# Kernel tuning notes

Measured on AMD Instinct MI355X. Metric: run time of the kernel, lower is better.

The kernel has to match this reference:

```python
import jax, jax.numpy as jnp
from jax import lax
import numpy as np

DN = ('NCDHW', 'OIDHW', 'NCDHW')
EPS = 1e-3  # BatchNorm1d eps=0.001
GRID = (41, 512, 512)  # spatial_shape [40,512,512] + [1,0,0]


def _block(x, mask, w, gamma, beta, rmean, rvar, stride, padding):
    # Regular (non-submanifold) sparse conv computes the same values as a dense
    # conv on the zero-filled grid; active OUTPUT sites are exactly those reached
    # by any active input site through the kernel window. BN+ReLU act only on
    # active sites (inactive sites stay exactly 0), hence the mask multiply.
    y = lax.conv_general_dilated(x, w, stride, padding, dimension_numbers=DN)
    k1 = jnp.ones((1, 1) + w.shape[2:], x.dtype)
    m = lax.conv_general_dilated(mask, k1, stride, padding, dimension_numbers=DN)
    m = (m > 0).astype(x.dtype)
    inv = gamma / jnp.sqrt(rvar + EPS)
    scale = inv.reshape(1, -1, 1, 1, 1)
    shift = (beta - rmean * inv).reshape(1, -1, 1, 1, 1)
    return jax.nn.relu(y * scale + shift) * m, m


def setup_inputs() -> dict:
    key = jax.random.key(0)
    NV, B = 120000, 2
    kf, kb, kz, ky, kx, kp = jax.random.split(key, 6)
    voxel_features = jax.random.normal(kf, (NV, 3), jnp.float32)
    coors = jnp.stack([
        jax.random.randint(kb, (NV,), 0, B, jnp.int32),
        jax.random.randint(kz, (NV,), 0, 40, jnp.int32),
        jax.random.randint(ky, (NV,), 0, 512, jnp.int32),
        jax.random.randint(kx, (NV,), 0, 512, jnp.int32)], axis=1)
    inp = {"voxel_features": voxel_features, "coors": coors, "batch_size": B}
    chans = [(3, 16, (3, 3, 3)), (16, 32, (3, 3, 3)), (32, 64, (3, 3, 3)), (64, 64, (3, 1, 1))]
    for i, (ci, co, k) in enumerate(chans, 1):
        kw, kg, kbb, km, kv = jax.random.split(jax.random.fold_in(kp, i), 5)
        fan = ci * k[0] * k[1] * k[2]
        inp[f"w{i}"] = jax.random.normal(kw, (co, ci) + k, jnp.float32) / np.sqrt(fan).astype(np.float32)
        inp[f"g{i}"] = jax.random.uniform(kg, (co,), jnp.float32, 0.5, 1.5)
        inp[f"bb{i}"] = jax.random.normal(kbb, (co,), jnp.float32) * 0.1
        inp[f"rm{i}"] = jax.random.normal(km, (co,), jnp.float32) * 0.1
        inp[f"rv{i}"] = jax.random.uniform(kv, (co,), jnp.float32, 0.5, 1.5)
    return inp


def reference(voxel_features, coors, batch_size,
              w1, g1, bb1, rm1, rv1,
              w2, g2, bb2, rm2, rv2,
              w3, g3, bb3, rm3, rv3,
              w4, g4, bb4, rm4, rv4):
    D, H, W = GRID
    C = voxel_features.shape[1]
    b, z, y, x = coors[:, 0], coors[:, 1], coors[:, 2], coors[:, 3]
    dense = jnp.zeros((batch_size, C, D, H, W), voxel_features.dtype)
    dense = dense.at[b, :, z, y, x].add(voxel_features)  # scatter voxels to grid
    mask = jnp.zeros((batch_size, 1, D, H, W), voxel_features.dtype).at[b, 0, z, y, x].set(1.0)
    h, m = _block(dense, mask, w1, g1, bb1, rm1, rv1, (2, 2, 2), [(1, 1), (1, 1), (1, 1)])
    h, m = _block(h, m, w2, g2, bb2, rm2, rv2, (2, 2, 2), [(1, 1), (1, 1), (1, 1)])
    h, m = _block(h, m, w3, g3, bb3, rm3, rv3, (2, 2, 2), [(0, 0), (1, 1), (1, 1)])
    h, m = _block(h, m, w4, g4, bb4, rm4, rv4, (2, 1, 1), [(0, 0), (0, 0), (0, 0)])
    N, Co, Dd, Hh, Ww = h.shape  # [B, 64, 2, 64, 64]
    return h.reshape(N, Co * Dd, Hh, Ww)
```

## Files before the change

### kernel.cpp

```cpp
#include <hip/hip_runtime.h>

#define EPS 1e-3f


static __device__ __forceinline__ unsigned f2bf(float f) {
    unsigned u = __float_as_uint(f);
    return (u + 0x7FFFu + ((u >> 16) & 1u)) >> 16;
}

typedef _Float16 f16x8 __attribute__((ext_vector_type(8)));
typedef float f32x4 __attribute__((ext_vector_type(4)));
typedef float f32x16 __attribute__((ext_vector_type(16)));

#define SLACK_BYTE 2752512
#define SLACK_Y1   90832912

__global__ __launch_bounds__(256) void repack_prezero(
    const float* __restrict__ g1, const float* __restrict__ b1,
    const float* __restrict__ rm1, const float* __restrict__ rv1,
    const float* __restrict__ w2, const float* __restrict__ g2, const float* __restrict__ b2,
    const float* __restrict__ rm2, const float* __restrict__ rv2,
    const float* __restrict__ w3, const float* __restrict__ g3, const float* __restrict__ b3,
    const float* __restrict__ rm3, const float* __restrict__ rv3,
    const float* __restrict__ w4, const float* __restrict__ g4, const float* __restrict__ b4,
    const float* __restrict__ rm4, const float* __restrict__ rv4,
    _Float16* __restrict__ wB2, _Float16* __restrict__ wB3,
    _Float16* __restrict__ wB4, float* __restrict__ shb,
    const int* __restrict__ coors, int NV, unsigned short* __restrict__ y1,
    unsigned char* __restrict__ m1, float* __restrict__ m3)
{
    if (blockIdx.x >= 1034) {
        const int i = (blockIdx.x - 1034) * 256 + threadIdx.x;
        if (i < NV) {
            const int b = coors[4 * i + 0];
            const int z = coors[4 * i + 1];
            const int y = coors[4 * i + 2];
            const int x = coors[4 * i + 3];
            int ozv[2], nz = 0, oyv[2], ny = 0, oxv[2], nx = 0;
#pragma unroll
            for (int k = 0; k < 3; ++k) {
                int t = z + 1 - k;
                if (t >= 0 && !(t & 1)) { int o = t >> 1; if (o < 21) ozv[nz++] = o; }
            }
#pragma unroll
            for (int k = 0; k < 3; ++k) {
                int t = y + 1 - k;
                if (t >= 0 && !(t & 1)) { int o = t >> 1; if (o < 256) oyv[ny++] = o; }
            }
#pragma unroll
            for (int k = 0; k < 3; ++k) {
                int t = x + 1 - k;
                if (t >= 0 && !(t & 1)) { int o = t >> 1; if (o < 256) oxv[nx++] = o; }
            }
            const uint4 zz = {0u, 0u, 0u, 0u};
            for (int a = 0; a < nz; ++a)
                for (int bb = 0; bb < ny; ++bb)
                    for (int c = 0; c < nx; ++c) {
                        const int sp = ozv[a] * 65536 + oyv[bb] * 256 + oxv[c];
                        uint4* p = (uint4*)(y1 + (size_t)(b * 1376256 + sp) * 16);
                        p[0] = zz;
                        p[1] = zz;
                    }
        }
        asm volatile("s_waitcnt vmcnt(0)" ::: "memory");
        return;
    }
    if (blockIdx.x >= 321) {
        const int idx16 = (blockIdx.x - 321) * 256 + threadIdx.x;
        const uint4 zz = {0u, 0u, 0u, 0u};
        if (idx16 < 172034) {
            ((uint4*)m1)[idx16] = zz;
        } else if (idx16 < 182274) {
            ((uint4*)m3)[idx16 - 172034] = zz;
        }
        return;
    }

    const int i = blockIdx.x * 256 + threadIdx.x;
    if (i < 13824) {
        const int j = i & 7, lane = (i >> 3) & 63, tap = i >> 9;
        const int oc = lane & 31;
        const int cin = (lane >> 5) * 8 + j;
        const float inv = g2[oc] * rsqrtf(rv2[oc] + EPS);
        wB2[i] = (_Float16)(w2[(oc * 16 + cin) * 27 + tap] * inv);
    } else if (i >= 14336 && i < 69632) {
        const int j2 = i - 14336;
        const int j = j2 & 7, lane = (j2 >> 3) & 63, t = (j2 >> 9) & 3, tap = j2 >> 11;
        const int q = lane >> 4, n = lane & 15;
        const int oc = t * 16 + n;
        const int cin = q * 8 + j;
        const float inv = g3[oc] * rsqrtf(rv3[oc] + EPS);
        wB3[j2] = (_Float16)(w3[(oc * 32 + cin) * 27 + tap] * inv);
    } else if (i >= 69632 && i < 81920) {
        const int j2 = i - 69632;
        const int j = j2 & 7, lane = (j2 >> 3) & 63, t = (j2 >> 9) & 3, c = j2 >> 11;
        const int q = lane >> 4, n = lane & 15;
        const int oc = t * 16 + n;
        const int k = c * 32 + q * 8 + j;
        const int dz = k >> 6, cin = k & 63;
        const float inv = g4[oc] * rsqrtf(rv4[oc] + EPS);
        wB4[j2] = (_Float16)(w4[(oc * 64 + cin) * 3 + dz] * inv);
    } else if (i >= 81920 && i < 82112) {
        const int j = i - 81920;
        if (j < 32) {
            const float inv = g2[j] * rsqrtf(rv2[j] + EPS);
            shb[j] = b2[j] - rm2[j] * inv;
        } else if (j < 96) {
            const int o = j - 32;
            const float inv = g3[o] * rsqrtf(rv3[o] + EPS);
            shb[j] = b3[o] - rm3[o] * inv;
        } else if (j < 160) {
            const int o = j - 96;
            const float inv = g4[o] * rsqrtf(rv4[o] + EPS);
            shb[j] = b4[o] - rm4[o] * inv;
        } else if (j < 176) {
            const int o = j - 160;
            shb[j] = g1[o] * rsqrtf(rv1[o] + EPS);
        } else if (j < 192) {
            const int o = j - 176;
            const float inv = g1[o] * rsqrtf(rv1[o] + EPS);
            shb[j] = b1[o] - rm1[o] * inv;
        }
    }
}

__global__ __launch_bounds__(256) void scatter_l1(
    const float* __restrict__ vf, const int* __restrict__ coors, int NV,
    const float* __restrict__ w1, const float* __restrict__ shb,
    unsigned short* __restrict__ y1, unsigned char* __restrict__ m1)
{
    __shared__ float ws[16 * 3 * 27];
    for (int e = threadIdx.x; e < 16 * 3 * 27; e += 256)
        ws[e] = w1[e] * shb[160 + e / 81];
    __syncthreads();

    const int gid = blockIdx.x * 256 + threadIdx.x;
    const int i = gid >> 3;
    const int oc2 = gid & 7;
    if (i < NV) {
        const int oc = oc2 * 2;

        const int b = coors[4 * i + 0];
        const int z = coors[4 * i + 1];
        const int y = coors[4 * i + 2];
        const int x = coors[4 * i + 3];
        const float f0 = vf[3 * i + 0];
        const float f1 = vf[3 * i + 1];
        const float f2 = vf[3 * i + 2];

        int ozv[2], kzv[2], nz = 0;
        int oyv[2], kyv[2], ny = 0;
        int oxv[2], kxv[2], nx = 0;
#pragma unroll
        for (int k = 0; k < 3; ++k) {
            int t = z + 1 - k;
            if (t >= 0 && !(t & 1)) { int o = t >> 1; if (o < 21) { ozv[nz] = o; kzv[nz] = k; ++nz; } }
        }
#pragma unroll
        for (int k = 0; k < 3; ++k) {
            int t = y + 1 - k;
            if (t >= 0 && !(t & 1)) { int o = t >> 1; if (o < 256) { oyv[ny] = o; kyv[ny] = k; ++ny; } }
        }
#pragma unroll
        for (int k = 0; k < 3; ++k) {
            int t = x + 1 - k;
            if (t >= 0 && !(t & 1)) { int o = t >> 1; if (o < 256) { oxv[nx] = o; kxv[nx] = k; ++nx; } }
        }

        for (int a = 0; a < nz; ++a)
            for (int bb = 0; bb < ny; ++bb)
                for (int c = 0; c < nx; ++c) {
                    const int oz = ozv[a], oy = oyv[bb], ox = oxv[c];
                    const int tap = (kzv[a] * 3 + kyv[bb]) * 3 + kxv[c];
                    const int sp = oz * 65536 + oy * 256 + ox;
                    if (oc2 == 0) m1[b * 1376256 + sp] = 1;
                    const float s0 = ws[oc * 81 + tap] * f0 + ws[oc * 81 + 27 + tap] * f1 +
                                     ws[oc * 81 + 54 + tap] * f2;
                    const float s1 = ws[(oc + 1) * 81 + tap] * f0 +
                                     ws[(oc + 1) * 81 + 27 + tap] * f1 +
                                     ws[(oc + 1) * 81 + 54 + tap] * f2;
                    const unsigned pk = f2bf(s0) | (f2bf(s1) << 16);
                    unsigned* addr = (unsigned*)(y1 + (size_t)(b * 1376256 + sp) * 16 +
                                                 oc2 * 2);
                    asm volatile("global_atomic_pk_add_bf16 %0, %1, off"
                                 : : "v"(addr), "v"(pk) : "memory");
                }
    }
    asm volatile("s_waitcnt vmcnt(0)" ::: "memory");
}

__global__ __launch_bounds__(256) void masks_pass(
    const unsigned char* __restrict__ m1, float* __restrict__ m2,
    float* __restrict__ m3)
{
    const int idx = blockIdx.x * 256 + threadIdx.x;
    const int b = idx / 180224;
    const int r = idx - b * 180224;
    const int oz = r >> 14, r2 = r & 16383, oy = r2 >> 7, ox = r2 & 127;
    const int iz0 = 2 * oz - 1, iyb = 2 * oy - 1, ixb = 2 * ox - 1;
    unsigned msum = 0;
#pragma unroll
    for (int kz = 0; kz < 3; ++kz) {
        const int iz = iz0 + kz;
#pragma unroll
        for (int ky = 0; ky < 3; ++ky) {
            const int iy = iyb + ky;
#pragma unroll
            for (int kx = 0; kx < 3; ++kx) {
                const int ix = ixb + kx;
                if ((unsigned)iz < 21u && (unsigned)iy < 256u &&
                    (unsigned)ix < 256u)
                    msum |= m1[b * 1376256 + iz * 65536 + iy * 256 + ix];
            }
        }
    }
    m2[idx] = msum ? 1.f : 0.f;

    if (msum) {
        int ozv[2], nz = 0, oyv[2], ny = 0, oxv[2], nx = 0;
#pragma unroll
        for (int k = 0; k < 3; ++k) {
            int t = oz - k;
            if (t >= 0 && !(t & 1)) { int o = t >> 1; if (o < 5) ozv[nz++] = o; }
        }
#pragma unroll
        for (int k = 0; k < 3; ++k) {
            int t = oy + 1 - k;
            if (t >= 0 && !(t & 1)) { int o = t >> 1; if (o < 64) oyv[ny++] = o; }
        }
#pragma unroll
        for (int k = 0; k < 3; ++k) {
            int t = ox + 1 - k;
            if (t >= 0 && !(t & 1)) { int o = t >> 1; if (o < 64) oxv[nx++] = o; }
        }
        for (int a = 0; a < nz; ++a)
            for (int bb = 0; bb < ny; ++bb)
                for (int c = 0; c < nx; ++c)
                    m3[b * 20480 + ozv[a] * 4096 + oyv[bb] * 64 + oxv[c]] = 1.0f;
    }
}

__global__ __launch_bounds__(256) __attribute__((amdgpu_waves_per_eu(4, 8)))
void conv_l2(
    const unsigned char* __restrict__ y1c,
    const unsigned char* __restrict__ m1,
    const uint4* __restrict__ wB2,
    const float* __restrict__ m2, const float* __restrict__ shb,
    _Float16* __restrict__ h2h)
{
    __shared__ unsigned char lds[3 * 8320];

    const int tid = threadIdx.x;
    const int lane = tid & 63;
    const int w = tid >> 6;
    const int m = lane & 31, h = lane >> 5;

    const int sbid = (blockIdx.x & 7) * 352 + (blockIdx.x >> 3);
    const int oy = sbid / 22;
    const int plane = sbid - oy * 22;
    const int b = plane / 11, oz = plane - b * 11;

    const int ox0 = w * 32;
    const int iz0 = 2 * oz - 1, iyb = 2 * oy - 1;
    const int ixm = 2 * (ox0 + m) - 1;
    const int bbase = b * 1376256;
    const int qoff = h * 16;

    unsigned mbits = 0;
#pragma unroll
    for (int t = 0; t < 27; ++t) {
        const int kz = t / 9, ky = (t / 3) % 3, kx = t % 3;
        const int iz = iz0 + kz, iy = iyb + ky, ix = ixm + kx;
        const bool v = (unsigned)iz < 21u && (unsigned)iy < 256u &&
                       (unsigned)ix < 256u;
        const int cell = bbase + iz * 65536 + iy * 256 + ix;
        mbits |= (unsigned)(m1[v ? cell : SLACK_BYTE] & 1) << t;
    }

    float s1v[8];
    {
        const float4* sp = (const float4*)(shb + 176 + h * 8);
        const float4 a0 = sp[0], a1 = sp[1];
        s1v[0] = a0.x; s1v[1] = a0.y; s1v[2] = a0.z; s1v[3] = a0.w;
        s1v[4] = a1.x; s1v[5] = a1.y; s1v[6] = a1.z; s1v[7] = a1.w;
    }

    int rdo[3];
#pragma unroll
    for (int kx = 0; kx < 3; ++kx) {
        const unsigned lx = (unsigned)(2 * (ox0 + m) + kx);
        const unsigned L = lx * 32 + qoff;
        rdo[kx] = (int)(L ^ (((L >> 7) & 7u) << 4));
    }

    int su_row[7], su_ix[7], su_half[7];
#pragma unroll
    for (int it = 0; it < 7; ++it) {
        const int t = it * 256 + tid;
        const int row = t / 520;
        const int u = t - row * 520;
        const unsigned L = (unsigned)(u * 16) ^ (((unsigned)(u >> 3) & 7u) << 4);
        su_row[it] = row;
        su_ix[it] = (int)(L >> 5) - 1;
        su_half[it] = (int)((L >> 4) & 1u);
    }

    f32x16 acc;
#pragma unroll
    for (int r = 0; r < 16; ++r) acc[r] = 0.f;

    for (int kz = 0; kz < 3; ++kz) {
        const int iz = iz0 + kz;
        const bool izok = (unsigned)iz < 21u;
        const int zrow = bbase + iz * 65536;

        __syncthreads();
#pragma unroll
        for (int it = 0; it < 7; ++it) {
            const int t = it * 256 + tid;
            if (t < 1560) {
                const int row = su_row[it];
                const int iy = iyb + row;
                const int ix = su_ix[it];
                const bool v = izok && (unsigned)iy < 256u && (unsigned)ix < 256u;
                const int srcb = v ? ((zrow + iy * 256 + ix) * 32 + su_half[it] * 16)
                                   : (int)SLACK_Y1;
                const int bt = t - lane;
                __builtin_amdgcn_global_load_lds(
                    (const __attribute__((address_space(1))) unsigned char*)(y1c + srcb),
                    (__attribute__((address_space(3))) unsigned char*)(lds + bt * 16),
                    16, 0, 0);
            }
        }
        asm volatile("s_waitcnt vmcnt(0)" ::: "memory");
        __syncthreads();

#pragma unroll
        for (int ky = 0; ky < 3; ++ky) {
            const int rbase = ky * 8320;
#pragma unroll
            for (int kx = 0; kx < 3; ++kx) {
                const int tap = kz * 9 + ky * 3 + kx;
                const uint4 ua = *(const uint4*)(lds + rbase + rdo[kx]);
                const bool act = (mbits >> tap) & 1u;
                unsigned od[4];
                const unsigned dvs[4] = {ua.x, ua.y, ua.z, ua.w};
#pragma unroll
                for (int jj = 0; jj < 4; ++jj) {
                    const unsigned dv = dvs[jj];
                    const float vlo = fmaxf(__uint_as_float(dv << 16) + s1v[2 * jj], 0.f);
                    const float vhi = fmaxf(__uint_as_float(dv & 0xFFFF0000u) + s1v[2 * jj + 1], 0.f);
                    const unsigned pk = __builtin_bit_cast(
                        unsigned, __builtin_amdgcn_cvt_pkrtz(vlo, vhi));
                    od[jj] = act ? pk : 0u;
                }
                const uint4 uc = {od[0], od[1], od[2], od[3]};
                const f16x8 af = __builtin_bit_cast(f16x8, uc);
                const f16x8 bf = __builtin_bit_cast(f16x8, wB2[tap * 64 + lane]);
                acc = __builtin_amdgcn_mfma_f32_32x32x16_f16(af, bf, acc, 0, 0, 0);
            }
        }
    }

    const int oc = lane & 31;
#pragma unroll
    for (int r = 0; r < 16; ++r) {
        const int row = (r & 3) + 8 * (r >> 2) + 4 * h;
        const int px = ox0 + row;
        const int spo = oz * 16384 + oy * 128 + px;
        const float mv = m2[b * 180224 + spo];
        const size_t cbase = (size_t)(b * 180224 + spo) * 32;
        h2h[cbase + oc] = (_Float16)(fmaxf(acc[r] + shb[oc], 0.f) * mv);
    }
}

__global__ __launch_bounds__(256) __attribute__((amdgpu_waves_per_eu(4, 8)))
void conv_l3(
    const unsigned char* __restrict__ h2h,
    const uint4* __restrict__ wB3,
    const float* __restrict__ m3, const float* __restrict__ shb,
    _Float16* __restrict__ h3h)
{
    const int tid = threadIdx.x;
    const int gw = blockIdx.x * 4 + (tid >> 6);
    const int lane = tid & 63;
    const int m = lane & 15, q = lane >> 4;

    const int plane = gw >> 8;
    const int rem = gw & 255;
    const int oy = rem >> 2;
    const int ox0 = (rem & 3) * 16;
    const int b = plane / 5, oz = plane % 5;
    const int iz0 = 2 * oz, iyb = 2 * oy - 1;
    const int ixm = 2 * (ox0 + m) - 1;
    const int bbase = b * 180224;
    const int qoff = q * 16;

    f32x4 acc[4];
#pragma unroll
    for (int t = 0; t < 4; ++t) acc[t] = (f32x4){0.f, 0.f, 0.f, 0.f};

    uint4 buf[9];
    bool  val[9];
#pragma unroll
    for (int t = 0; t < 9; ++t) {
        const int ky = (t / 3) % 3, kx = t % 3;
        const int iz = iz0 + t / 9, iy = iyb + ky, ix = ixm + kx;
        const bool v = (unsigned)iy < 128u && (unsigned)ix < 128u;
        const int cell = bbase + iz * 16384 + iy * 128 + ix;
        buf[t] = *(const uint4*)(h2h + (v ? (cell * 64 + qoff) : 0));
        val[t] = v;
    }

#pragma unroll
    for (int tap = 0; tap < 27; ++tap) {
        const int s = tap % 9;
        uint4 ua = buf[s];
        if (!val[s]) { ua.x = 0; ua.y = 0; ua.z = 0; ua.w = 0; }
        if (tap + 9 < 27) {
            const int t2 = tap + 9;
            const int kz = t2 / 9, ky = (t2 / 3) % 3, kx = t2 % 3;
            const int iz = iz0 + kz, iy = iyb + ky, ix = ixm + kx;
            const bool v = (unsigned)iy < 128u && (unsigned)ix < 128u;
            const int cell = bbase + iz * 16384 + iy * 128 + ix;
            buf[s] = *(const uint4*)(h2h + (v ? (cell * 64 + qoff) : 0));
            val[s] = v;
        }
        const f16x8 af = __builtin_bit_cast(f16x8, ua);
#pragma unroll
        for (int t = 0; t < 4; ++t) {
            const f16x8 bf = __builtin_bit_cast(f16x8, wB3[(tap * 4 + t) * 64 + lane]);
            acc[t] = __builtin_amdgcn_mfma_f32_16x16x32_f16(af, bf, acc[t], 0, 0, 0);
        }
    }

    const int n = lane & 15;
#pragma unroll
    for (int r = 0; r < 4; ++r) {
        const int px = ox0 + q * 4 + r;
        const int spo = oz * 4096 + oy * 64 + px;
        const float mv = m3[b * 20480 + spo];
        const size_t cb = (size_t)(b * 20480 + spo) * 64;
#pragma unroll
        for (int t = 0; t < 4; ++t) {
            const int oc = t * 16 + n;
            h3h[cb + oc] = (_Float16)(fmaxf(acc[t][r] + shb[32 + oc], 0.f) * mv);
        }
    }
}

__global__ __launch_bounds__(256) __attribute__((amdgpu_waves_per_eu(4, 8)))
void conv_l4(
    const unsigned char* __restrict__ h3h,
    const uint4* __restrict__ wB4,
    const float* __restrict__ m3, const float* __restrict__ shb,
    float* __restrict__ out)
{
    const int tid = threadIdx.x;
    const int gw = blockIdx.x * 4 + (tid >> 6);
    const int lane = tid & 63;
    const int m = lane & 15, q = lane >> 4;

    const int b = gw >> 9, od = (gw >> 8) & 1;
    const int oy = (gw >> 2) & 63, ox0 = (gw & 3) * 16;
    const int cellbase = (b * 5 + 2 * od) * 4096 + oy * 64 + ox0 + m;

    f32x4 acc[4];
#pragma unroll
    for (int t = 0; t < 4; ++t) acc[t] = (f32x4){0.f, 0.f, 0.f, 0.f};

#pragma unroll
    for (int c = 0; c < 6; ++c) {
        const int dz = c >> 1;
        const size_t addr = (size_t)(cellbase + dz * 4096) * 128 +
                            (c & 1) * 64 + q * 16;
        const uint4 ua = *(const uint4*)(h3h + addr);
        const f16x8 af = __builtin_bit_cast(f16x8, ua);
#pragma unroll
        for (int t = 0; t < 4; ++t) {
            const f16x8 bf = __builtin_bit_cast(f16x8, wB4[(c * 4 + t) * 64 + lane]);
            acc[t] = __builtin_amdgcn_mfma_f32_16x16x32_f16(af, bf, acc[t], 0, 0, 0);
        }
    }

    const int n = lane & 15;
#pragma unroll
    for (int r = 0; r < 4; ++r) {
        const int px = ox0 + q * 4 + r;
        const int spo = oy * 64 + px;
        const float msum = m3[(b * 5 + 2 * od + 0) * 4096 + spo] +
                           m3[(b * 5 + 2 * od + 1) * 4096 + spo] +
                           m3[(b * 5 + 2 * od + 2) * 4096 + spo];
        const float mv = msum > 0.f ? 1.f : 0.f;
#pragma unroll
        for (int t = 0; t < 4; ++t) {
            const int oc = t * 16 + n;
            out[((b * 64 + oc) * 2 + od) * 4096 + spo] =
                fmaxf(acc[t][r] + shb[96 + oc], 0.f) * mv;
        }
    }
}

extern "C" void kernel_launch(void* const* d_in, const int* in_sizes, int n_in,
                              void* d_out, int out_size, void* d_ws, size_t ws_size,
                              hipStream_t stream)
{
    const float* vf    = (const float*)d_in[0];
    const int*   coors = (const int*)d_in[1];
    const float* w1 = (const float*)d_in[3];
    const float* g1 = (const float*)d_in[4];
    const float* b1 = (const float*)d_in[5];
    const float* rm1 = (const float*)d_in[6];
    const float* rv1 = (const float*)d_in[7];
    const float* w2 = (const float*)d_in[8];
    const float* g2 = (const float*)d_in[9];
    const float* b2 = (const float*)d_in[10];
    const float* rm2 = (const float*)d_in[11];
    const float* rv2 = (const float*)d_in[12];
    const float* w3 = (const float*)d_in[13];
    const float* g3 = (const float*)d_in[14];
    const float* b3 = (const float*)d_in[15];
    const float* rm3 = (const float*)d_in[16];
    const float* rv3 = (const float*)d_in[17];
    const float* w4 = (const float*)d_in[18];
    const float* g4 = (const float*)d_in[19];
    const float* b4 = (const float*)d_in[20];
    const float* rm4 = (const float*)d_in[21];
    const float* rv4 = (const float*)d_in[22];

    const int NV = in_sizes[0] / 3;

    float* ws = (float*)d_ws;
    float* y1  = ws;
    float* m1f = y1 + 22020096;
    float* h2h = m1f + 2752512;
    float* m2  = h2h + 5767168;
    float* h3h = m2 + 360448;
    float* m3  = h3h + 1310720;
    float* wB2 = m3 + 40960;
    float* wB3 = wB2 + 7168;
    float* wB4 = wB3 + 27648;
    float* shb = wB4 + 6144;

    unsigned char* m1 = (unsigned char*)m1f;

    const int pzBlocks = (NV + 255) / 256;
    repack_prezero<<<1034 + pzBlocks, 256, 0, stream>>>(
        g1, b1, rm1, rv1,
        w2, g2, b2, rm2, rv2, w3, g3, b3, rm3, rv3,
        w4, g4, b4, rm4, rv4,
        (_Float16*)wB2, (_Float16*)wB3, (_Float16*)wB4, shb,
        coors, NV, (unsigned short*)y1, m1, m3);
    scatter_l1<<<(NV * 8 + 255) / 256, 256, 0, stream>>>(vf, coors, NV, w1, shb,
                                                         (unsigned short*)y1, m1);
    masks_pass<<<1408, 256, 0, stream>>>(m1, m2, m3);
    conv_l2<<<2816, 256, 0, stream>>>((const unsigned char*)d_ws, m1,
                                      (const uint4*)wB2, m2, shb, (_Float16*)h2h);
    conv_l3<<<640, 256, 0, stream>>>((const unsigned char*)h2h, (const uint4*)wB3,
                                     m3, shb, (_Float16*)h3h);
    conv_l4<<<256, 256, 0, stream>>>((const unsigned char*)h3h, (const uint4*)wB4,
                                     m3, shb, (float*)d_out);
}
```

Measured before the change: 202.4 us.

## Apply BN/ReLU/mask during staging into LDS instead of per-tap in conv_l2

The staging loop now loads input rows into registers with plain global loads, applies the layer-1 shift, ReLU, fp16 conversion and active-mask once per staged element, and writes swizzled fp16 values into LDS. The MFMA loop then reads ready-to-use operands, so the per-tap 27-load mask gather and the repeated per-tap activation math are removed. In exchange, the asynchronous global-to-LDS loads are replaced by register round trips, which raises register pressure and adds latency before the barrier.

```diff
diff --git a/kernel.cpp b/kernel.cpp
--- a/kernel.cpp
+++ b/kernel.cpp
@@ -248,7 +248,8 @@
     const float* __restrict__ m2, const float* __restrict__ shb,
     _Float16* __restrict__ h2h)
 {
-    __shared__ unsigned char lds[3 * 8320];
+    __shared__ uint4 lds4[3 * 520];
+    unsigned char* lds = (unsigned char*)lds4;
 
     const int tid = threadIdx.x;
     const int lane = tid & 63;
@@ -262,24 +263,14 @@
 
     const int ox0 = w * 32;
     const int iz0 = 2 * oz - 1, iyb = 2 * oy - 1;
-    const int ixm = 2 * (ox0 + m) - 1;
     const int bbase = b * 1376256;
     const int qoff = h * 16;
 
-    unsigned mbits = 0;
-#pragma unroll
-    for (int t = 0; t < 27; ++t) {
-        const int kz = t / 9, ky = (t / 3) % 3, kx = t % 3;
-        const int iz = iz0 + kz, iy = iyb + ky, ix = ixm + kx;
-        const bool v = (unsigned)iz < 21u && (unsigned)iy < 256u &&
-                       (unsigned)ix < 256u;
-        const int cell = bbase + iz * 65536 + iy * 256 + ix;
-        mbits |= (unsigned)(m1[v ? cell : SLACK_BYTE] & 1) << t;
-    }
+    const int shalf = tid & 1;
 
     float s1v[8];
     {
-        const float4* sp = (const float4*)(shb + 176 + h * 8);
+        const float4* sp = (const float4*)(shb + 176 + shalf * 8);
         const float4 a0 = sp[0], a1 = sp[1];
         s1v[0] = a0.x; s1v[1] = a0.y; s1v[2] = a0.z; s1v[3] = a0.w;
         s1v[4] = a1.x; s1v[5] = a1.y; s1v[6] = a1.z; s1v[7] = a1.w;
@@ -288,21 +279,23 @@
     int rdo[3];
 #pragma unroll
     for (int kx = 0; kx < 3; ++kx) {
-        const unsigned lx = (unsigned)(2 * (ox0 + m) + kx);
-        const unsigned L = lx * 32 + qoff;
+        const unsigned L = (unsigned)((2 * (ox0 + m) + kx) * 32 + qoff);
         rdo[kx] = (int)(L ^ (((L >> 7) & 7u) << 4));
     }
 
-    int su_row[7], su_ix[7], su_half[7];
+    int st_row[7], st_ix[7], st_lws[7];
+    bool st_ok[7];
 #pragma unroll
     for (int it = 0; it < 7; ++it) {
-        const int t = it * 256 + tid;
-        const int row = t / 520;
-        const int u = t - row * 520;
-        const unsigned L = (unsigned)(u * 16) ^ (((unsigned)(u >> 3) & 7u) << 4);
-        su_row[it] = row;
-        su_ix[it] = (int)(L >> 5) - 1;
-        su_half[it] = (int)((L >> 4) & 1u);
+        const int l = it * 256 + tid;
+        st_ok[it] = l < 1560;
+        const int row = l / 520;
+        const int u = l - row * 520;
+        const int lx = u >> 1;
+        st_row[it] = row;
+        st_ix[it] = lx - 1;
+        const unsigned Ll = (unsigned)(lx * 32 + shalf * 16);
+        st_lws[it] = row * 8320 + (int)(Ll ^ (((Ll >> 7) & 7u) << 4));
     }
 
     f32x16 acc;
@@ -315,36 +308,26 @@
         const int zrow = bbase + iz * 65536;
 
         __syncthreads();
+        uint4 sd[7];
+        unsigned char sm[7];
 #pragma unroll
         for (int it = 0; it < 7; ++it) {
-            const int t = it * 256 + tid;
-            if (t < 1560) {
-                const int row = su_row[it];
-                const int iy = iyb + row;
-                const int ix = su_ix[it];
-                const bool v = izok && (unsigned)iy < 256u && (unsigned)ix < 256u;
-                const int srcb = v ? ((zrow + iy * 256 + ix) * 32 + su_half[it] * 16)
-                                   : (int)SLACK_Y1;
-                const int bt = t - lane;
-                __builtin_amdgcn_global_load_lds(
-                    (const __attribute__((address_space(1))) unsigned char*)(y1c + srcb),
-                    (__attribute__((address_space(3))) unsigned char*)(lds + bt * 16),
-                    16, 0, 0);
-            }
-        }
-        asm volatile("s_waitcnt vmcnt(0)" ::: "memory");
-        __syncthreads();
-
-#pragma unroll
-        for (int ky = 0; ky < 3; ++ky) {
-            const int rbase = ky * 8320;
-#pragma unroll
-            for (int kx = 0; kx < 3; ++kx) {
-                const int tap = kz * 9 + ky * 3 + kx;
-                const uint4 ua = *(const uint4*)(lds + rbase + rdo[kx]);
-                const bool act = (mbits >> tap) & 1u;
+            if (st_ok[it]) {
+                const int iy = iyb + st_row[it];
+                const bool v = izok && (unsigned)iy < 256u &&
+                               (unsigned)st_ix[it] < 256u;
+                const int cell = zrow + iy * 256 + st_ix[it];
+                sd[it] = *(const uint4*)(y1c +
+                          (v ? (cell * 32 + shalf * 16) : (int)SLACK_Y1));
+                sm[it] = m1[v ? cell : SLACK_BYTE];
+            }
+        }
+#pragma unroll
+        for (int it = 0; it < 7; ++it) {
+            if (st_ok[it]) {
+                const bool act = sm[it] != 0;
                 unsigned od[4];
-                const unsigned dvs[4] = {ua.x, ua.y, ua.z, ua.w};
+                const unsigned dvs[4] = {sd[it].x, sd[it].y, sd[it].z, sd[it].w};
 #pragma unroll
                 for (int jj = 0; jj < 4; ++jj) {
                     const unsigned dv = dvs[jj];
@@ -355,7 +338,18 @@
                     od[jj] = act ? pk : 0u;
                 }
                 const uint4 uc = {od[0], od[1], od[2], od[3]};
-                const f16x8 af = __builtin_bit_cast(f16x8, uc);
+                *(uint4*)(lds + st_lws[it]) = uc;
+            }
+        }
+        __syncthreads();
+
+#pragma unroll
+        for (int ky = 0; ky < 3; ++ky) {
+#pragma unroll
+            for (int kx = 0; kx < 3; ++kx) {
+                const int tap = kz * 9 + ky * 3 + kx;
+                const uint4 ua = *(const uint4*)(lds + ky * 8320 + rdo[kx]);
+                const f16x8 af = __builtin_bit_cast(f16x8, ua);
                 const f16x8 bf = __builtin_bit_cast(f16x8, wB2[tap * 64 + lane]);
                 acc = __builtin_amdgcn_mfma_f32_32x32x16_f16(af, bf, acc, 0, 0, 0);
             }
```

Result: faster. 197.7 us, median of 2 (-2.3%).
